# Performance work log

Hardware: AMD Instinct MI355X
Metric: run time of the kernel (lower is better)

Reference implementation:

```python
import jax, jax.numpy as jnp
import numpy as np

DIM = 64
N_EMBED = 512


def setup_inputs() -> dict:
    key = jax.random.key(0)
    k_x, k_e = jax.random.split(key)
    x = jax.random.normal(k_x, (32, 64, 64, DIM), dtype=jnp.float32)
    # codebook buffer: embed has shape [dim, n_embed] as in the torch module
    embed = jax.random.normal(k_e, (DIM, N_EMBED), dtype=jnp.float32)
    return {"x": x, "embed": embed}


def reference(x, embed):
    # x: [B, H, W, dim]; embed: [dim, n_embed]
    dim = embed.shape[0]
    flat = x.reshape(-1, dim)  # [N, dim]
    # squared euclidean distance (same argmin as torch.cdist's euclid dist)
    # d2[n, k] = ||flat[n]||^2 - 2 flat[n].embed[:,k] + ||embed[:,k]||^2
    d2 = (
        jnp.sum(flat * flat, axis=1, keepdims=True)
        - 2.0 * (flat @ embed)
        + jnp.sum(embed * embed, axis=0)[None, :]
    )  # [N, n_embed]
    embed_ind = jnp.argmin(d2, axis=1)  # [N]
    embed_ind = embed_ind.reshape(x.shape[:-1])  # [B, H, W]
    # embedding lookup from embed.T ([n_embed, dim])
    quantize = jnp.take(embed.T, embed_ind, axis=0)  # [B, H, W, dim]
    diff = jnp.mean(jnp.square(jax.lax.stop_gradient(quantize) - x))
    # straight-through estimator
    quantize_st = x + jax.lax.stop_gradient(quantize - x)
    return quantize_st, diff, embed_ind
```

## Files before the change

kernel.cpp:

```cpp
#include <hip/hip_runtime.h>


#define DIM      64
#define NCODE    512
#define NVEC     (32 * 64 * 64)
#define WAVES    4
#define BLK      256
#define NCT      16
#define CHUNK_DW 3072

typedef unsigned int u32;
typedef __attribute__((ext_vector_type(8)))  short bf16x8;
typedef __attribute__((ext_vector_type(16))) float f32x16;

#define GLOAD_LDS16(gp, lp)                                                      \
  __builtin_amdgcn_global_load_lds(                                              \
      (const __attribute__((address_space(1))) u32*)(gp),                        \
      (__attribute__((address_space(3))) u32*)(lp), 16, 0, 0)

__device__ __forceinline__ void split3(float v, u32& h, u32& m, u32& lo) {
    const u32 u = __float_as_uint(v);
    h = u >> 16;
    const float r1 = v - __uint_as_float(u & 0xFFFF0000u);
    const u32 u1 = __float_as_uint(r1);
    m = u1 >> 16;
    const float r2 = r1 - __uint_as_float(u1 & 0xFFFF0000u);
    lo = __float_as_uint(r2) >> 16;
}

__global__ void vq_prep(const float* __restrict__ embed,
                        u32* __restrict__ bfrag,
                        float* __restrict__ et,
                        float* __restrict__ norms) {
    const int tg = blockIdx.x * BLK + threadIdx.x;
    {
        const int ct = tg >> 6, l = tg & 63;
        const int c = ct * 32 + (l & 31), kh = l >> 5;
        double nsum = 0.0;
        u32 w[3][4][4];
        #pragma unroll
        for (int s = 0; s < 4; ++s) {
            float v[8];
            #pragma unroll
            for (int j = 0; j < 8; ++j) {
                const int d = 16 * s + kh * 8 + j;
                v[j] = embed[d * NCODE + c];
                nsum += (double)v[j] * (double)v[j];
            }
            #pragma unroll
            for (int q = 0; q < 4; ++q) {
                u32 h0, m0, l0, h1, m1, l1;
                split3(v[2 * q], h0, m0, l0);
                split3(v[2 * q + 1], h1, m1, l1);
                w[0][s][q] = h0 | (h1 << 16);
                w[1][s][q] = m0 | (m1 << 16);
                w[2][s][q] = l0 | (l1 << 16);
            }
        }
        const double tot = nsum + __shfl_xor(nsum, 32, 64);
        if (kh == 0) norms[c] = (float)tot;
        #pragma unroll
        for (int p = 0; p < 3; ++p) {
            #pragma unroll
            for (int s = 0; s < 4; ++s) {
                u32* dst = bfrag + ct * CHUNK_DW + (p * 4 + s) * 256 + l * 4;
                *reinterpret_cast<uint4*>(dst) =
                    make_uint4(w[p][s][0], w[p][s][1], w[p][s][2], w[p][s][3]);
            }
        }
    }
    {
        const int c = tg >> 1, dh = (tg & 1) * 32;
        float buf[32];
        #pragma unroll
        for (int i = 0; i < 32; ++i) buf[i] = embed[(dh + i) * NCODE + c];
        #pragma unroll
        for (int i = 0; i < 8; ++i)
            *reinterpret_cast<float4*>(et + c * DIM + dh + i * 4) =
                make_float4(buf[4 * i], buf[4 * i + 1], buf[4 * i + 2], buf[4 * i + 3]);
    }
}

__global__ __launch_bounds__(BLK, 3) void vq_main(
        const float* __restrict__ x,
        const u32* __restrict__ bfrag,
        const float* __restrict__ et,
        const float* __restrict__ norms,
        float* __restrict__ out) {
    __shared__ u32 lbuf[2][CHUNK_DW];
    __shared__ float lnorm[NCODE];
    __shared__ int sbk[WAVES][32];
    __shared__ float red[WAVES];

    const int tid = threadIdx.x;
    const int wid = tid >> 6, l = tid & 63;
    const int rl = l & 31, kh = l >> 5;
    const int n0 = (blockIdx.x * WAVES + wid) * 32;

    for (int i = tid; i < NCODE; i += BLK) lnorm[i] = norms[i];

    bf16x8 afr[3][4];
    {
        const float* xp = x + (size_t)(n0 + rl) * DIM + kh * 8;
        #pragma unroll
        for (int s = 0; s < 4; ++s) {
            const float4 va = *reinterpret_cast<const float4*>(xp + 16 * s);
            const float4 vb = *reinterpret_cast<const float4*>(xp + 16 * s + 4);
            const float v[8] = {va.x, va.y, va.z, va.w, vb.x, vb.y, vb.z, vb.w};
            #pragma unroll
            for (int q = 0; q < 4; ++q) {
                u32 h0, m0, l0, h1, m1, l1;
                split3(v[2 * q], h0, m0, l0);
                split3(v[2 * q + 1], h1, m1, l1);
                afr[0][s][2 * q] = (short)h0;  afr[0][s][2 * q + 1] = (short)h1;
                afr[1][s][2 * q] = (short)m0;  afr[1][s][2 * q + 1] = (short)m1;
                afr[2][s][2 * q] = (short)l0;  afr[2][s][2 * q + 1] = (short)l1;
            }
        }
    }

    {
        const u32* gsrc = bfrag + wid * 256 + (l << 2);
        u32* lp = &lbuf[0][wid * 256];
        #pragma unroll
        for (int i = 0; i < 3; ++i) GLOAD_LDS16(gsrc + i * 1024, lp + i * 1024);
    }
    __syncthreads();

    float best[16];
    int bk[16];
    #pragma unroll
    for (int r = 0; r < 16; ++r) { best[r] = __builtin_inff(); bk[r] = 0; }

    int cur = 0;
    for (int ct = 0; ct < NCT; ++ct) {
        if (ct + 1 < NCT) {
            const u32* gsrc = bfrag + (ct + 1) * CHUNK_DW + wid * 256 + (l << 2);
            u32* lp = &lbuf[cur ^ 1][wid * 256];
            #pragma unroll
            for (int i = 0; i < 3; ++i) GLOAD_LDS16(gsrc + i * 1024, lp + i * 1024);
        }

        f32x16 acc;
        #pragma unroll
        for (int r = 0; r < 16; ++r) acc[r] = 0.0f;

        const int l4 = l << 2;
        #pragma unroll
        for (int s = 0; s < 4; ++s) {
            const bf16x8 bh = *reinterpret_cast<const bf16x8*>(&lbuf[cur][(0 * 4 + s) * 256 + l4]);
            const bf16x8 bm = *reinterpret_cast<const bf16x8*>(&lbuf[cur][(1 * 4 + s) * 256 + l4]);
            const bf16x8 bl = *reinterpret_cast<const bf16x8*>(&lbuf[cur][(2 * 4 + s) * 256 + l4]);
            acc = __builtin_amdgcn_mfma_f32_32x32x16_bf16(afr[0][s], bh, acc, 0, 0, 0);
            acc = __builtin_amdgcn_mfma_f32_32x32x16_bf16(afr[0][s], bm, acc, 0, 0, 0);
            acc = __builtin_amdgcn_mfma_f32_32x32x16_bf16(afr[1][s], bh, acc, 0, 0, 0);
            acc = __builtin_amdgcn_mfma_f32_32x32x16_bf16(afr[1][s], bm, acc, 0, 0, 0);
            acc = __builtin_amdgcn_mfma_f32_32x32x16_bf16(afr[0][s], bl, acc, 0, 0, 0);
            acc = __builtin_amdgcn_mfma_f32_32x32x16_bf16(afr[2][s], bh, acc, 0, 0, 0);
        }

        const int col = ct * 32 + rl;
        const float nrm = lnorm[col];
        #pragma unroll
        for (int r = 0; r < 16; ++r) {
            const float sc = fmaf(-2.0f, acc[r], nrm);
            if (sc < best[r]) { best[r] = sc; bk[r] = col; }
        }

        __syncthreads();
        cur ^= 1;
    }

    #pragma unroll
    for (int off = 1; off <= 16; off <<= 1) {
        #pragma unroll
        for (int r = 0; r < 16; ++r) {
            const float ob = __shfl_xor(best[r], off, 64);
            const int obk  = __shfl_xor(bk[r], off, 64);
            if (ob < best[r] || (ob == best[r] && obk < bk[r])) { best[r] = ob; bk[r] = obk; }
        }
    }
    if (rl == 0) {
        #pragma unroll
        for (int r = 0; r < 16; ++r) sbk[wid][(r & 3) + 8 * (r >> 2) + 4 * kh] = bk[r];
    }

    float dp = 0.0f;
    const int rsub = l >> 4;
    const int dcol = (l & 15) * 4;
    #pragma unroll
    for (int i = 0; i < 8; ++i) {
        const int row = i * 4 + rsub;
        const int k = sbk[wid][row];
        const float4 q  = *reinterpret_cast<const float4*>(et + k * DIM + dcol);
        const float4 xv = *reinterpret_cast<const float4*>(x + (size_t)(n0 + row) * DIM + dcol);
        *reinterpret_cast<float4*>(out + (size_t)(n0 + row) * DIM + dcol) = q;
        const float d0 = q.x - xv.x, d1 = q.y - xv.y, d2 = q.z - xv.z, d3 = q.w - xv.w;
        dp = fmaf(d0, d0, dp); dp = fmaf(d1, d1, dp);
        dp = fmaf(d2, d2, dp); dp = fmaf(d3, d3, dp);
    }
    if (l < 32) out[(size_t)NVEC * DIM + 1 + n0 + l] = (float)sbk[wid][l];

    #pragma unroll
    for (int off = 32; off >= 1; off >>= 1) dp += __shfl_down(dp, off, 64);
    if (l == 0) red[wid] = dp;
    __syncthreads();
    if (tid == 0) {
        const float s = (red[0] + red[1]) + (red[2] + red[3]);
        atomicAdd(out + (size_t)NVEC * DIM, s * (1.0f / ((float)NVEC * (float)DIM)));
    }
}

extern "C" void kernel_launch(void* const* d_in, const int* in_sizes, int n_in,
                              void* d_out, int out_size, void* d_ws, size_t ws_size,
                              hipStream_t stream) {
    const float* x     = (const float*)d_in[0];
    const float* embed = (const float*)d_in[1];
    float* out = (float*)d_out;

    u32* bfrag   = (u32*)d_ws;
    float* et    = (float*)d_ws + NCT * CHUNK_DW;
    float* norms = et + (size_t)NCODE * DIM;

    hipMemsetAsync((char*)d_out + (size_t)NVEC * DIM * sizeof(float), 0,
                   sizeof(float), stream);

    vq_prep<<<4, BLK, 0, stream>>>(embed, bfrag, et, norms);
    vq_main<<<NVEC / (WAVES * 32), BLK, 0, stream>>>(x, bfrag, et, norms, out);
}
```

Before: 137.0 us.

## Parallelize codebook prep, drop memset, and use manual vmcnt barriers in main loop

The prep kernel now runs across 16 blocks, with one thread per 8-element slice producing the bf16 split fragments, transposed codebook and norms in a single pass. It also zeroes the loss accumulator, removing the separate memset call. The main kernel issues its first codebook prefetch before the x split work, raises occupancy hints to 4 blocks per SM, and replaces __syncthreads with explicit vmcnt waits plus raw s_barrier. The hand-written waits risk missing LDS write visibility for the norms table if the compiler does not add lgkmcnt waits.

Result: no change. 134.4 us (-1.9%).

```diff
diff --git a/kernel.cpp b/kernel.cpp
--- a/kernel.cpp
+++ b/kernel.cpp
@@ -31,63 +31,57 @@
 __global__ void vq_prep(const float* __restrict__ embed,
                         u32* __restrict__ bfrag,
                         float* __restrict__ et,
-                        float* __restrict__ norms) {
-    const int tg = blockIdx.x * BLK + threadIdx.x;
-    {
-        const int ct = tg >> 6, l = tg & 63;
-        const int c = ct * 32 + (l & 31), kh = l >> 5;
-        double nsum = 0.0;
-        u32 w[3][4][4];
-        #pragma unroll
-        for (int s = 0; s < 4; ++s) {
-            float v[8];
-            #pragma unroll
-            for (int j = 0; j < 8; ++j) {
-                const int d = 16 * s + kh * 8 + j;
-                v[j] = embed[d * NCODE + c];
-                nsum += (double)v[j] * (double)v[j];
-            }
-            #pragma unroll
-            for (int q = 0; q < 4; ++q) {
-                u32 h0, m0, l0, h1, m1, l1;
-                split3(v[2 * q], h0, m0, l0);
-                split3(v[2 * q + 1], h1, m1, l1);
-                w[0][s][q] = h0 | (h1 << 16);
-                w[1][s][q] = m0 | (m1 << 16);
-                w[2][s][q] = l0 | (l1 << 16);
-            }
-        }
-        const double tot = nsum + __shfl_xor(nsum, 32, 64);
-        if (kh == 0) norms[c] = (float)tot;
-        #pragma unroll
-        for (int p = 0; p < 3; ++p) {
-            #pragma unroll
-            for (int s = 0; s < 4; ++s) {
-                u32* dst = bfrag + ct * CHUNK_DW + (p * 4 + s) * 256 + l * 4;
-                *reinterpret_cast<uint4*>(dst) =
-                    make_uint4(w[p][s][0], w[p][s][1], w[p][s][2], w[p][s][3]);
-            }
-        }
-    }
-    {
-        const int c = tg >> 1, dh = (tg & 1) * 32;
-        float buf[32];
-        #pragma unroll
-        for (int i = 0; i < 32; ++i) buf[i] = embed[(dh + i) * NCODE + c];
-        #pragma unroll
-        for (int i = 0; i < 8; ++i)
-            *reinterpret_cast<float4*>(et + c * DIM + dh + i * 4) =
-                make_float4(buf[4 * i], buf[4 * i + 1], buf[4 * i + 2], buf[4 * i + 3]);
-    }
-}
-
-__global__ __launch_bounds__(BLK, 3) void vq_main(
+                        float* __restrict__ norms,
+                        float* __restrict__ out) {
+    const int gid = blockIdx.x * BLK + threadIdx.x;
+    const int c = gid >> 3, g = gid & 7;
+    const int s = g >> 1, kh = g & 1;
+
+    float v[8];
+    double ns = 0.0;
+    #pragma unroll
+    for (int j = 0; j < 8; ++j) {
+        v[j] = embed[(16 * s + 8 * kh + j) * NCODE + c];
+        ns += (double)v[j] * (double)v[j];
+    }
+    ns += __shfl_xor(ns, 1, 64);
+    ns += __shfl_xor(ns, 2, 64);
+    ns += __shfl_xor(ns, 4, 64);
+    if (g == 0) norms[c] = (float)ns;
+
+    u32 wH[4], wM[4], wL[4];
+    #pragma unroll
+    for (int q = 0; q < 4; ++q) {
+        u32 h0, m0, l0, h1, m1, l1;
+        split3(v[2 * q], h0, m0, l0);
+        split3(v[2 * q + 1], h1, m1, l1);
+        wH[q] = h0 | (h1 << 16);
+        wM[q] = m0 | (m1 << 16);
+        wL[q] = l0 | (l1 << 16);
+    }
+    const int ct = c >> 5, lb = (c & 31) + 32 * kh;
+    u32* base = bfrag + ct * CHUNK_DW;
+    *reinterpret_cast<uint4*>(base + (0 * 4 + s) * 256 + lb * 4) =
+        make_uint4(wH[0], wH[1], wH[2], wH[3]);
+    *reinterpret_cast<uint4*>(base + (1 * 4 + s) * 256 + lb * 4) =
+        make_uint4(wM[0], wM[1], wM[2], wM[3]);
+    *reinterpret_cast<uint4*>(base + (2 * 4 + s) * 256 + lb * 4) =
+        make_uint4(wL[0], wL[1], wL[2], wL[3]);
+
+    float* ep = et + c * DIM + 16 * s + 8 * kh;
+    *reinterpret_cast<float4*>(ep)     = make_float4(v[0], v[1], v[2], v[3]);
+    *reinterpret_cast<float4*>(ep + 4) = make_float4(v[4], v[5], v[6], v[7]);
+
+    if (gid == 0) out[(size_t)NVEC * DIM] = 0.0f;
+}
+
+__global__ __launch_bounds__(BLK, 4) void vq_main(
         const float* __restrict__ x,
         const u32* __restrict__ bfrag,
         const float* __restrict__ et,
         const float* __restrict__ norms,
         float* __restrict__ out) {
-    __shared__ u32 lbuf[2][CHUNK_DW];
+    __shared__ __align__(16) u32 lbuf[2][CHUNK_DW];
     __shared__ float lnorm[NCODE];
     __shared__ int sbk[WAVES][32];
     __shared__ float red[WAVES];
@@ -97,6 +91,13 @@
     const int rl = l & 31, kh = l >> 5;
     const int n0 = (blockIdx.x * WAVES + wid) * 32;
 
+    {
+        const u32* gsrc = bfrag + wid * 256 + (l << 2);
+        u32* lp = &lbuf[0][wid * 256];
+        GLOAD_LDS16(gsrc, lp);
+        GLOAD_LDS16(gsrc + 1024, lp + 1024);
+        GLOAD_LDS16(gsrc + 2048, lp + 2048);
+    }
     for (int i = tid; i < NCODE; i += BLK) lnorm[i] = norms[i];
 
     bf16x8 afr[3][4];
@@ -119,27 +120,24 @@
         }
     }
 
-    {
-        const u32* gsrc = bfrag + wid * 256 + (l << 2);
-        u32* lp = &lbuf[0][wid * 256];
-        #pragma unroll
-        for (int i = 0; i < 3; ++i) GLOAD_LDS16(gsrc + i * 1024, lp + i * 1024);
-    }
-    __syncthreads();
-
     float best[16];
     int bk[16];
     #pragma unroll
     for (int r = 0; r < 16; ++r) { best[r] = __builtin_inff(); bk[r] = 0; }
 
-    int cur = 0;
     for (int ct = 0; ct < NCT; ++ct) {
+        const int cur = ct & 1;
         if (ct + 1 < NCT) {
             const u32* gsrc = bfrag + (ct + 1) * CHUNK_DW + wid * 256 + (l << 2);
             u32* lp = &lbuf[cur ^ 1][wid * 256];
-            #pragma unroll
-            for (int i = 0; i < 3; ++i) GLOAD_LDS16(gsrc + i * 1024, lp + i * 1024);
-        }
+            GLOAD_LDS16(gsrc, lp);
+            GLOAD_LDS16(gsrc + 1024, lp + 1024);
+            GLOAD_LDS16(gsrc + 2048, lp + 2048);
+            asm volatile("s_waitcnt vmcnt(3)" ::: "memory");
+        } else {
+            asm volatile("s_waitcnt vmcnt(0)" ::: "memory");
+        }
+        asm volatile("s_barrier" ::: "memory");
 
         f32x16 acc;
         #pragma unroll
@@ -167,8 +165,7 @@
             if (sc < best[r]) { best[r] = sc; bk[r] = col; }
         }
 
-        __syncthreads();
-        cur ^= 1;
+        asm volatile("s_barrier" ::: "memory");
     }
 
     #pragma unroll
@@ -222,9 +219,6 @@
     float* et    = (float*)d_ws + NCT * CHUNK_DW;
     float* norms = et + (size_t)NCODE * DIM;
 
-    hipMemsetAsync((char*)d_out + (size_t)NVEC * DIM * sizeof(float), 0,
-                   sizeof(float), stream);
-
-    vq_prep<<<4, BLK, 0, stream>>>(embed, bfrag, et, norms);
+    vq_prep<<<16, BLK, 0, stream>>>(embed, bfrag, et, norms, out);
     vq_main<<<NVEC / (WAVES * 32), BLK, 0, stream>>>(x, bfrag, et, norms, out);
 }
```
